# Optimization experiments

Hardware: AMD Instinct MI355X
Metric: run time of the kernel (lower is better)

Reference implementation:

```python
import jax, jax.numpy as jnp
import numpy as np

U, I, D = 50000, 25000, 128          # users, items, emb_size
E = 1_000_000                        # user-item interactions
L = 3                                # num_layers
B = 4096                             # BPR batch size
N = U + I                            # total graph nodes


def setup_inputs() -> dict:
    key = jax.random.key(0)
    k1, k2, k3, k4, k5, k6, k7 = jax.random.split(key, 7)
    # Xavier-ish embedding tables
    user_emb = jax.random.normal(k1, (U, D), jnp.float32) * 0.1
    item_emb = jax.random.normal(k2, (I, D), jnp.float32) * 0.1
    # random bipartite interactions -> symmetric COO adjacency over N nodes
    eu = jax.random.randint(k3, (E,), 0, U)            # user node ids
    ei = jax.random.randint(k4, (E,), 0, I) + U        # item node ids (offset)
    adj_row = jnp.concatenate([eu, ei]).astype(jnp.int32)   # [2E]
    adj_col = jnp.concatenate([ei, eu]).astype(jnp.int32)   # [2E]
    # symmetric normalization D^-1/2 A D^-1/2 (matches create_adj_mat)
    deg = jax.ops.segment_sum(jnp.ones(2 * E, jnp.float32), adj_row, num_segments=N)
    d_inv = jnp.where(deg > 0, deg ** -0.5, 0.0)
    adj_vals = d_inv[adj_row] * d_inv[adj_col]               # [2E] float32
    users = jax.random.randint(k5, (B,), 0, U).astype(jnp.int32)
    pos_items = jax.random.randint(k6, (B,), 0, I).astype(jnp.int32)
    neg_items = jax.random.randint(k7, (B,), 0, I).astype(jnp.int32)
    return dict(user_emb=user_emb, item_emb=item_emb, adj_row=adj_row,
                adj_col=adj_col, adj_vals=adj_vals, users=users,
                pos_items=pos_items, neg_items=neg_items)


def _spmm(vals, row, col, x):
    # sparse [N,N] @ dense [N,D] via gather + segment_sum
    return jax.ops.segment_sum(vals[:, None] * x[col], row, num_segments=N)


def reference(user_emb, item_emb, adj_row, adj_col, adj_vals,
              users, pos_items, neg_items):
    ego = jnp.concatenate([user_emb, item_emb], axis=0)      # [N, D]
    # FAITHFUL to the torch source: ego_embeddings is never reassigned inside
    # the layer loop, so every one of the L layer outputs equals A @ ego.
    # mean(stack([ego, A@ego, ..., A@ego])) == (ego + L * A@ego) / (L + 1)
    h = _spmm(adj_vals, adj_row, adj_col, ego)               # [N, D]
    final = (ego + L * h) / (L + 1)                          # mean over L+1 layers
    u_final = final[:U]
    i_final = final[U:]
    u_g = u_final[users]                                     # [B, D]
    pos_i_g = i_final[pos_items]                             # [B, D]
    neg_i_g = i_final[neg_items]                             # [B, D]
    return (u_g, pos_i_g, neg_i_g, i_final)
```

## Files before the change

### kernel.cpp

```cpp
#include <hip/hip_runtime.h>
#include <hip/hip_bf16.h>

#define U_CNT 50000
#define I_CNT 25000
#define D_DIM 128
#define E_CNT 1000000
#define B_CNT 4096
#define ICAP 96
#define UCAP 64
#define PNCAP 16
#define BM_WORDS 1600
#define IRANGE (I_CNT / 8)
#define URANGE (U_CNT / 8)
#define NGROUP 1000
#define CHUNK  (E_CNT / NGROUP)


__device__ __forceinline__ unsigned pack_bf2(float lo, float hi) {
    __hip_bfloat16 a = __float2bfloat16(lo);
    __hip_bfloat16 b = __float2bfloat16(hi);
    unsigned short ua = *reinterpret_cast<unsigned short*>(&a);
    unsigned short ub = *reinterpret_cast<unsigned short*>(&b);
    return ((unsigned)ub << 16) | ua;
}
__device__ __forceinline__ float bf_lo(unsigned w) { return __uint_as_float(w << 16); }
__device__ __forceinline__ float bf_hi(unsigned w) { return __uint_as_float(w & 0xffff0000u); }

__global__ __launch_bounds__(256) void prep_kernel(
        const float* __restrict__ user_emb,
        const int*   __restrict__ users,
        const int*   __restrict__ pos_items,
        const int*   __restrict__ neg_items,
        unsigned*    __restrict__ ue16,
        unsigned*    __restrict__ bitmap,
        int*         __restrict__ slot,
        int*         __restrict__ pncnt,
        int*         __restrict__ pnbuck) {
    const int i = blockIdx.x * blockDim.x + threadIdx.x;
    if (i < U_CNT * 64) {
        const float2 f = ((const float2*)user_emb)[i];
        ue16[i] = pack_bf2(f.x, f.y);
    }
    if (i < B_CNT) {
        const int u = users[i];
        atomicOr(&bitmap[u >> 5], 1u << (u & 31));
        atomicCAS(&slot[u], 0, i + 1);
    }
    if (i < 2 * B_CNT) {
        const int idx = (i < B_CNT) ? pos_items[i] : neg_items[i - B_CNT];
        const int c = atomicAdd(&pncnt[idx], 1);
        if (c < PNCAP) pnbuck[idx * PNCAP + c] = B_CNT + i;
    }
}

__global__ __launch_bounds__(256) void bucket_kernel(
        const int*      __restrict__ adj_row,
        const int*      __restrict__ adj_col,
        const float*    __restrict__ adj_vals,
        const unsigned* __restrict__ bitmap,
        const int*      __restrict__ slot,
        int*  __restrict__ icnt,  int*  __restrict__ ucnt,
        int2* __restrict__ ibuck, int2* __restrict__ ubuck) {
    const unsigned x = blockIdx.x & 7;
    const int      g = blockIdx.x >> 3;
    const int base = g * CHUNK + (int)threadIdx.x * 4;
    if (base >= g * CHUNK + CHUNK) return;

    const int4   uu = *(const int4*)  (adj_row  + base);
    const int4   tt = *(const int4*)  (adj_col  + base);
    const float4 vv = *(const float4*)(adj_vals + base);
    const unsigned us[4] = {(unsigned)uu.x, (unsigned)uu.y,
                            (unsigned)uu.z, (unsigned)uu.w};
    const unsigned ts[4] = {(unsigned)(tt.x - U_CNT), (unsigned)(tt.y - U_CNT),
                            (unsigned)(tt.z - U_CNT), (unsigned)(tt.w - U_CNT)};
    const float    vs[4] = {vv.x, vv.y, vv.z, vv.w};

#pragma unroll
    for (int k = 0; k < 4; ++k) {
        const unsigned u = us[k], t = ts[k];
        const int vb = __float_as_int(vs[k]);
        if (t / IRANGE == x) {
            const int c = atomicAdd(&icnt[t], 1);
            ibuck[(size_t)t * ICAP + c] = make_int2((int)u, vb);
        }
        if (u / URANGE == x) {
            if ((bitmap[u >> 5] >> (u & 31)) & 1u) {
                const int j0 = slot[u] - 1;
                const int c2 = atomicAdd(&ucnt[j0], 1);
                ubuck[(size_t)j0 * UCAP + c2] = make_int2((int)t, vb);
            }
        }
    }
}

__global__ __launch_bounds__(256) void gather_kernel(
        const float*    __restrict__ user_emb,
        const float*    __restrict__ item_emb,
        const unsigned* __restrict__ ue16,
        const int*      __restrict__ users,
        const int*      __restrict__ slot,
        const int*      __restrict__ icnt,
        const int*      __restrict__ ucnt,
        const int*      __restrict__ pncnt,
        const int*      __restrict__ pnbuck,
        const int2*     __restrict__ ibuck,
        const int2*     __restrict__ ubuck,
        float*          __restrict__ out) {
    const int lane = threadIdx.x & 63;
    const int w    = (blockIdx.x * blockDim.x + threadIdx.x) >> 6;

    if (w < I_CNT) {
        const int t = w;
        const int   n = icnt[t];
        const int2* b = ibuck + (size_t)t * ICAP;
        float ax = 0.0f, ay = 0.0f;
        int p = 0;
        for (; p + 4 <= n; p += 4) {
            const int2 e0 = b[p], e1 = b[p+1], e2 = b[p+2], e3 = b[p+3];
            const unsigned w0 = ue16[(size_t)e0.x * 64 + lane];
            const unsigned w1 = ue16[(size_t)e1.x * 64 + lane];
            const unsigned w2 = ue16[(size_t)e2.x * 64 + lane];
            const unsigned w3 = ue16[(size_t)e3.x * 64 + lane];
            const float v0 = __int_as_float(e0.y), v1 = __int_as_float(e1.y);
            const float v2 = __int_as_float(e2.y), v3 = __int_as_float(e3.y);
            ax += v0*bf_lo(w0) + v1*bf_lo(w1) + v2*bf_lo(w2) + v3*bf_lo(w3);
            ay += v0*bf_hi(w0) + v1*bf_hi(w1) + v2*bf_hi(w2) + v3*bf_hi(w3);
        }
        for (; p < n; ++p) {
            const int2 e = b[p];
            const unsigned ww = ue16[(size_t)e.x * 64 + lane];
            const float v = __int_as_float(e.y);
            ax += v * bf_lo(ww);
            ay += v * bf_hi(ww);
        }
        const float2 eg = ((const float2*)(item_emb + (size_t)t * D_DIM))[lane];
        float2 o;
        o.x = (eg.x + 3.0f * ax) * 0.25f;
        o.y = (eg.y + 3.0f * ay) * 0.25f;
        ((float2*)(out + (size_t)(3 * B_CNT + t) * D_DIM))[lane] = o;
        const int pn = min(pncnt[t], PNCAP);
        for (int c = 0; c < pn; ++c) {
            const int row = pnbuck[t * PNCAP + c];
            ((float2*)(out + (size_t)row * D_DIM))[lane] = o;
        }
    } else if (w < I_CNT + B_CNT) {
        const int j  = w - I_CNT;
        const int u  = users[j];
        const int j0 = slot[u] - 1;
        const int   n = ucnt[j0];
        const int2* b = ubuck + (size_t)j0 * UCAP;
        float ax = 0.0f, ay = 0.0f;
        int p = 0;
        for (; p + 4 <= n; p += 4) {
            const int2 e0 = b[p], e1 = b[p+1], e2 = b[p+2], e3 = b[p+3];
            const float2 x0 = ((const float2*)(item_emb + (size_t)e0.x * D_DIM))[lane];
            const float2 x1 = ((const float2*)(item_emb + (size_t)e1.x * D_DIM))[lane];
            const float2 x2 = ((const float2*)(item_emb + (size_t)e2.x * D_DIM))[lane];
            const float2 x3 = ((const float2*)(item_emb + (size_t)e3.x * D_DIM))[lane];
            const float v0 = __int_as_float(e0.y), v1 = __int_as_float(e1.y);
            const float v2 = __int_as_float(e2.y), v3 = __int_as_float(e3.y);
            ax += v0*x0.x + v1*x1.x + v2*x2.x + v3*x3.x;
            ay += v0*x0.y + v1*x1.y + v2*x2.y + v3*x3.y;
        }
        for (; p < n; ++p) {
            const int2 e = b[p];
            const float2 xx = ((const float2*)(item_emb + (size_t)e.x * D_DIM))[lane];
            const float v = __int_as_float(e.y);
            ax += v * xx.x;
            ay += v * xx.y;
        }
        const float2 eg = ((const float2*)(user_emb + (size_t)u * D_DIM))[lane];
        float2 o;
        o.x = (eg.x + 3.0f * ax) * 0.25f;
        o.y = (eg.y + 3.0f * ay) * 0.25f;
        ((float2*)(out + (size_t)j * D_DIM))[lane] = o;
    }
}

extern "C" void kernel_launch(void* const* d_in, const int* in_sizes, int n_in,
                              void* d_out, int out_size, void* d_ws, size_t ws_size,
                              hipStream_t stream) {
    const float* user_emb  = (const float*)d_in[0];
    const float* item_emb  = (const float*)d_in[1];
    const int*   adj_row   = (const int*)  d_in[2];
    const int*   adj_col   = (const int*)  d_in[3];
    const float* adj_vals  = (const float*)d_in[4];
    const int*   users     = (const int*)  d_in[5];
    const int*   pos_items = (const int*)  d_in[6];
    const int*   neg_items = (const int*)  d_in[7];
    float* out = (float*)d_out;

    unsigned* bitmap = (unsigned*)d_ws;
    int* slot  = (int*)(bitmap + BM_WORDS);
    int* icnt  = slot + U_CNT;
    int* ucnt  = icnt + I_CNT;
    int* pncnt = ucnt + B_CNT;
    int2* ibuck = (int2*)(pncnt + I_CNT);
    int2* ubuck = ibuck + (size_t)I_CNT * ICAP;
    int*  pnbuck = (int*)(ubuck + (size_t)B_CNT * UCAP);
    unsigned* ue16 = (unsigned*)(pnbuck + (size_t)I_CNT * PNCAP);

    const size_t zero_ints = BM_WORDS + U_CNT + I_CNT + B_CNT + I_CNT;
    hipMemsetAsync(bitmap, 0, zero_ints * sizeof(int), stream);

    prep_kernel<<<(U_CNT * 64 + 255) / 256, 256, 0, stream>>>(
        user_emb, users, pos_items, neg_items, ue16, bitmap, slot, pncnt, pnbuck);

    bucket_kernel<<<NGROUP * 8, 256, 0, stream>>>(
        adj_row, adj_col, adj_vals, bitmap, slot, icnt, ucnt, ibuck, ubuck);

    gather_kernel<<<((I_CNT + B_CNT) * 64 + 255) / 256, 256, 0, stream>>>(
        user_emb, item_emb, ue16, users, slot, icnt, ucnt, pncnt, pnbuck,
        ibuck, ubuck, out);
}
```

Baseline: 209.6 us.

## Overlap bf16 user conversion with bucketing and widen item gather loads

The bf16 conversion of the user embedding table moves out of the prep kernel and into extra blocks of the bucketing kernel. This shrinks prep to a tiny launch and lets the conversion stream run concurrently with the atomic-heavy bucketing. The item-side gather now splits each wave into four 16-lane groups, each loading 16-byte rows of a different neighbor, then combines them with cross-lane shuffles. The goal is fewer, wider memory transactions and more independent loads in flight, at the cost of more registers and a shuffle reduction. Bucket counts are also clamped to their capacities.

```diff
diff --git a/kernel.cpp b/kernel.cpp
--- a/kernel.cpp
+++ b/kernel.cpp
@@ -14,6 +14,8 @@
 #define URANGE (U_CNT / 8)
 #define NGROUP 1000
 #define CHUNK  (E_CNT / NGROUP)
+#define BUCKET_BLKS (NGROUP * 8)
+#define CVT_BLKS 3125
 
 
 __device__ __forceinline__ unsigned pack_bf2(float lo, float hi) {
@@ -27,20 +29,14 @@
 __device__ __forceinline__ float bf_hi(unsigned w) { return __uint_as_float(w & 0xffff0000u); }
 
 __global__ __launch_bounds__(256) void prep_kernel(
-        const float* __restrict__ user_emb,
-        const int*   __restrict__ users,
-        const int*   __restrict__ pos_items,
-        const int*   __restrict__ neg_items,
-        unsigned*    __restrict__ ue16,
-        unsigned*    __restrict__ bitmap,
-        int*         __restrict__ slot,
-        int*         __restrict__ pncnt,
-        int*         __restrict__ pnbuck) {
+        const int* __restrict__ users,
+        const int* __restrict__ pos_items,
+        const int* __restrict__ neg_items,
+        unsigned*  __restrict__ bitmap,
+        int*       __restrict__ slot,
+        int*       __restrict__ pncnt,
+        int*       __restrict__ pnbuck) {
     const int i = blockIdx.x * blockDim.x + threadIdx.x;
-    if (i < U_CNT * 64) {
-        const float2 f = ((const float2*)user_emb)[i];
-        ue16[i] = pack_bf2(f.x, f.y);
-    }
     if (i < B_CNT) {
         const int u = users[i];
         atomicOr(&bitmap[u >> 5], 1u << (u & 31));
@@ -53,42 +49,53 @@
     }
 }
 
-__global__ __launch_bounds__(256) void bucket_kernel(
+__global__ __launch_bounds__(256) void bucket_cvt_kernel(
         const int*      __restrict__ adj_row,
         const int*      __restrict__ adj_col,
         const float*    __restrict__ adj_vals,
+        const float*    __restrict__ user_emb,
         const unsigned* __restrict__ bitmap,
         const int*      __restrict__ slot,
         int*  __restrict__ icnt,  int*  __restrict__ ucnt,
-        int2* __restrict__ ibuck, int2* __restrict__ ubuck) {
-    const unsigned x = blockIdx.x & 7;
-    const int      g = blockIdx.x >> 3;
-    const int base = g * CHUNK + (int)threadIdx.x * 4;
-    if (base >= g * CHUNK + CHUNK) return;
-
-    const int4   uu = *(const int4*)  (adj_row  + base);
-    const int4   tt = *(const int4*)  (adj_col  + base);
-    const float4 vv = *(const float4*)(adj_vals + base);
-    const unsigned us[4] = {(unsigned)uu.x, (unsigned)uu.y,
-                            (unsigned)uu.z, (unsigned)uu.w};
-    const unsigned ts[4] = {(unsigned)(tt.x - U_CNT), (unsigned)(tt.y - U_CNT),
-                            (unsigned)(tt.z - U_CNT), (unsigned)(tt.w - U_CNT)};
-    const float    vs[4] = {vv.x, vv.y, vv.z, vv.w};
-
+        int2* __restrict__ ibuck, int2* __restrict__ ubuck,
+        unsigned* __restrict__ ue16) {
+    if (blockIdx.x < BUCKET_BLKS) {
+        const unsigned x = blockIdx.x & 7;
+        const int      g = blockIdx.x >> 3;
+        const int base = g * CHUNK + (int)threadIdx.x * 4;
+        if (base >= g * CHUNK + CHUNK) return;
+
+        const int4   uu = *(const int4*)  (adj_row  + base);
+        const int4   tt = *(const int4*)  (adj_col  + base);
+        const float4 vv = *(const float4*)(adj_vals + base);
+        const unsigned us[4] = {(unsigned)uu.x, (unsigned)uu.y,
+                                (unsigned)uu.z, (unsigned)uu.w};
+        const unsigned ts[4] = {(unsigned)(tt.x - U_CNT), (unsigned)(tt.y - U_CNT),
+                                (unsigned)(tt.z - U_CNT), (unsigned)(tt.w - U_CNT)};
+        const float    vs[4] = {vv.x, vv.y, vv.z, vv.w};
 #pragma unroll
-    for (int k = 0; k < 4; ++k) {
-        const unsigned u = us[k], t = ts[k];
-        const int vb = __float_as_int(vs[k]);
-        if (t / IRANGE == x) {
-            const int c = atomicAdd(&icnt[t], 1);
-            ibuck[(size_t)t * ICAP + c] = make_int2((int)u, vb);
-        }
-        if (u / URANGE == x) {
-            if ((bitmap[u >> 5] >> (u & 31)) & 1u) {
-                const int j0 = slot[u] - 1;
-                const int c2 = atomicAdd(&ucnt[j0], 1);
-                ubuck[(size_t)j0 * UCAP + c2] = make_int2((int)t, vb);
-            }
+        for (int k = 0; k < 4; ++k) {
+            const unsigned u = us[k], t = ts[k];
+            const int vb = __float_as_int(vs[k]);
+            if (t / IRANGE == x) {
+                const int c = atomicAdd(&icnt[t], 1);
+                ibuck[(size_t)t * ICAP + c] = make_int2((int)u, vb);
+            }
+            if (u / URANGE == x) {
+                if ((bitmap[u >> 5] >> (u & 31)) & 1u) {
+                    const int j0 = slot[u] - 1;
+                    const int c2 = atomicAdd(&ucnt[j0], 1);
+                    ubuck[(size_t)j0 * UCAP + c2] = make_int2((int)t, vb);
+                }
+            }
+        }
+    } else {
+        const int bid = blockIdx.x - BUCKET_BLKS;
+        int i = bid * 1024 + threadIdx.x;
+#pragma unroll
+        for (int r = 0; r < 4; ++r, i += 256) {
+            const float2 f = ((const float2*)user_emb)[i];
+            ue16[i] = pack_bf2(f.x, f.y);
         }
     }
 }
@@ -110,49 +117,88 @@
     const int w    = (blockIdx.x * blockDim.x + threadIdx.x) >> 6;
 
     if (w < I_CNT) {
-        const int t = w;
-        const int   n = icnt[t];
+        const int t   = w;
+        const int n   = min(icnt[t], ICAP);
         const int2* b = ibuck + (size_t)t * ICAP;
-        float ax = 0.0f, ay = 0.0f;
-        int p = 0;
-        for (; p + 4 <= n; p += 4) {
-            const int2 e0 = b[p], e1 = b[p+1], e2 = b[p+2], e3 = b[p+3];
-            const unsigned w0 = ue16[(size_t)e0.x * 64 + lane];
-            const unsigned w1 = ue16[(size_t)e1.x * 64 + lane];
-            const unsigned w2 = ue16[(size_t)e2.x * 64 + lane];
-            const unsigned w3 = ue16[(size_t)e3.x * 64 + lane];
-            const float v0 = __int_as_float(e0.y), v1 = __int_as_float(e1.y);
-            const float v2 = __int_as_float(e2.y), v3 = __int_as_float(e3.y);
-            ax += v0*bf_lo(w0) + v1*bf_lo(w1) + v2*bf_lo(w2) + v3*bf_lo(w3);
-            ay += v0*bf_hi(w0) + v1*bf_hi(w1) + v2*bf_hi(w2) + v3*bf_hi(w3);
-        }
-        for (; p < n; ++p) {
-            const int2 e = b[p];
-            const unsigned ww = ue16[(size_t)e.x * 64 + lane];
+        const int sub = lane >> 4;
+        const int cl  = lane & 15;
+        float a0=0.f,a1=0.f,a2=0.f,a3=0.f,a4=0.f,a5=0.f,a6=0.f,a7=0.f;
+
+        int q = 0;
+        for (; q + 8 <= n; q += 8) {
+            const int2 eA = b[q + sub];
+            const int2 eB = b[q + 4 + sub];
+            const uint4 wA = *(const uint4*)(ue16 + (size_t)eA.x * 64 + cl * 4);
+            const uint4 wB = *(const uint4*)(ue16 + (size_t)eB.x * 64 + cl * 4);
+            const float vA = __int_as_float(eA.y), vB = __int_as_float(eB.y);
+            a0 += vA*bf_lo(wA.x) + vB*bf_lo(wB.x);
+            a1 += vA*bf_hi(wA.x) + vB*bf_hi(wB.x);
+            a2 += vA*bf_lo(wA.y) + vB*bf_lo(wB.y);
+            a3 += vA*bf_hi(wA.y) + vB*bf_hi(wB.y);
+            a4 += vA*bf_lo(wA.z) + vB*bf_lo(wB.z);
+            a5 += vA*bf_hi(wA.z) + vB*bf_hi(wB.z);
+            a6 += vA*bf_lo(wA.w) + vB*bf_lo(wB.w);
+            a7 += vA*bf_hi(wA.w) + vB*bf_hi(wB.w);
+        }
+        if (q + 4 <= n) {
+            const int2 e = b[q + sub];
+            const uint4 wv = *(const uint4*)(ue16 + (size_t)e.x * 64 + cl * 4);
             const float v = __int_as_float(e.y);
-            ax += v * bf_lo(ww);
-            ay += v * bf_hi(ww);
-        }
-        const float2 eg = ((const float2*)(item_emb + (size_t)t * D_DIM))[lane];
-        float2 o;
-        o.x = (eg.x + 3.0f * ax) * 0.25f;
-        o.y = (eg.y + 3.0f * ay) * 0.25f;
-        ((float2*)(out + (size_t)(3 * B_CNT + t) * D_DIM))[lane] = o;
-        const int pn = min(pncnt[t], PNCAP);
-        for (int c = 0; c < pn; ++c) {
-            const int row = pnbuck[t * PNCAP + c];
-            ((float2*)(out + (size_t)row * D_DIM))[lane] = o;
+            a0 += v*bf_lo(wv.x); a1 += v*bf_hi(wv.x);
+            a2 += v*bf_lo(wv.y); a3 += v*bf_hi(wv.y);
+            a4 += v*bf_lo(wv.z); a5 += v*bf_hi(wv.z);
+            a6 += v*bf_lo(wv.w); a7 += v*bf_hi(wv.w);
+            q += 4;
+        }
+        if (q < n) {
+            const int r = q + sub;
+            if (r < n) {
+                const int2 e = b[r];
+                const uint4 wv = *(const uint4*)(ue16 + (size_t)e.x * 64 + cl * 4);
+                const float v = __int_as_float(e.y);
+                a0 += v*bf_lo(wv.x); a1 += v*bf_hi(wv.x);
+                a2 += v*bf_lo(wv.y); a3 += v*bf_hi(wv.y);
+                a4 += v*bf_lo(wv.z); a5 += v*bf_hi(wv.z);
+                a6 += v*bf_lo(wv.w); a7 += v*bf_hi(wv.w);
+            }
+        }
+        a0 += __shfl_xor(a0, 16); a0 += __shfl_xor(a0, 32);
+        a1 += __shfl_xor(a1, 16); a1 += __shfl_xor(a1, 32);
+        a2 += __shfl_xor(a2, 16); a2 += __shfl_xor(a2, 32);
+        a3 += __shfl_xor(a3, 16); a3 += __shfl_xor(a3, 32);
+        a4 += __shfl_xor(a4, 16); a4 += __shfl_xor(a4, 32);
+        a5 += __shfl_xor(a5, 16); a5 += __shfl_xor(a5, 32);
+        a6 += __shfl_xor(a6, 16); a6 += __shfl_xor(a6, 32);
+        a7 += __shfl_xor(a7, 16); a7 += __shfl_xor(a7, 32);
+
+        if (sub == 0) {
+            const float* ie = item_emb + (size_t)t * D_DIM + cl * 8;
+            const float4 g0 = *(const float4*)(ie);
+            const float4 g1 = *(const float4*)(ie + 4);
+            float4 o0, o1;
+            o0.x = (g0.x + 3.0f*a0)*0.25f; o0.y = (g0.y + 3.0f*a1)*0.25f;
+            o0.z = (g0.z + 3.0f*a2)*0.25f; o0.w = (g0.w + 3.0f*a3)*0.25f;
+            o1.x = (g1.x + 3.0f*a4)*0.25f; o1.y = (g1.y + 3.0f*a5)*0.25f;
+            o1.z = (g1.z + 3.0f*a6)*0.25f; o1.w = (g1.w + 3.0f*a7)*0.25f;
+            float* orow = out + (size_t)(3 * B_CNT + t) * D_DIM + cl * 8;
+            *(float4*)orow = o0; *(float4*)(orow + 4) = o1;
+            const int pn = min(pncnt[t], PNCAP);
+            for (int c = 0; c < pn; ++c) {
+                const int row = pnbuck[t * PNCAP + c];
+                float* pr = out + (size_t)row * D_DIM + cl * 8;
+                *(float4*)pr = o0; *(float4*)(pr + 4) = o1;
+            }
         }
     } else if (w < I_CNT + B_CNT) {
         const int j  = w - I_CNT;
         const int u  = users[j];
         const int j0 = slot[u] - 1;
-        const int   n = ucnt[j0];
+        const int n  = min(ucnt[j0], UCAP);
         const int2* b = ubuck + (size_t)j0 * UCAP;
         float ax = 0.0f, ay = 0.0f;
-        int p = 0;
-        for (; p + 4 <= n; p += 4) {
-            const int2 e0 = b[p], e1 = b[p+1], e2 = b[p+2], e3 = b[p+3];
+        int q = 0;
+        for (; q + 4 <= n; q += 4) {
+            const int2 e0 = b[q], e1 = b[q+1], e2 = b[q+2], e3 = b[q+3];
             const float2 x0 = ((const float2*)(item_emb + (size_t)e0.x * D_DIM))[lane];
             const float2 x1 = ((const float2*)(item_emb + (size_t)e1.x * D_DIM))[lane];
             const float2 x2 = ((const float2*)(item_emb + (size_t)e2.x * D_DIM))[lane];
@@ -162,8 +208,8 @@
             ax += v0*x0.x + v1*x1.x + v2*x2.x + v3*x3.x;
             ay += v0*x0.y + v1*x1.y + v2*x2.y + v3*x3.y;
         }
-        for (; p < n; ++p) {
-            const int2 e = b[p];
+        for (; q < n; ++q) {
+            const int2 e = b[q];
             const float2 xx = ((const float2*)(item_emb + (size_t)e.x * D_DIM))[lane];
             const float v = __int_as_float(e.y);
             ax += v * xx.x;
@@ -203,13 +249,14 @@
     const size_t zero_ints = BM_WORDS + U_CNT + I_CNT + B_CNT + I_CNT;
     hipMemsetAsync(bitmap, 0, zero_ints * sizeof(int), stream);
 
-    prep_kernel<<<(U_CNT * 64 + 255) / 256, 256, 0, stream>>>(
-        user_emb, users, pos_items, neg_items, ue16, bitmap, slot, pncnt, pnbuck);
-
-    bucket_kernel<<<NGROUP * 8, 256, 0, stream>>>(
-        adj_row, adj_col, adj_vals, bitmap, slot, icnt, ucnt, ibuck, ubuck);
+    prep_kernel<<<(2 * B_CNT + 255) / 256, 256, 0, stream>>>(
+        users, pos_items, neg_items, bitmap, slot, pncnt, pnbuck);
+
+    bucket_cvt_kernel<<<BUCKET_BLKS + CVT_BLKS, 256, 0, stream>>>(
+        adj_row, adj_col, adj_vals, user_emb, bitmap, slot,
+        icnt, ucnt, ibuck, ubuck, ue16);
 
     gather_kernel<<<((I_CNT + B_CNT) * 64 + 255) / 256, 256, 0, stream>>>(
-        user_emb, item_emb, ue16, users, slot, icnt, ucnt, pncnt, pnbuck,
-        ibuck, ubuck, out);
-}
+        user_emb, item_emb, ue16, users, slot, icnt, ucnt,
+        pncnt, pnbuck, ibuck, ubuck, out);
+}
```

Measured after the change: 203.0 us. -3.1%, faster.
